# Kernel optimization log

Hardware: AMD Instinct MI355X
Metric: run time of the kernel (lower is better)

Reference implementation:

```python
import jax, jax.numpy as jnp
import numpy as np

N, E, F_IN, H, C = 20000, 320000, 256, 4, 64
D = H * C  # hidden_dim = 256
NEG_SLOPE = 0.2
LN_EPS = 1e-5


def setup_inputs() -> dict:
    key = jax.random.key(0)
    ks = jax.random.split(key, 12)
    x = jax.random.normal(ks[0], (N, F_IN), dtype=jnp.float32)
    # edges guaranteed self-loop-free (PyG GATConv removes then re-adds self loops)
    dst = jax.random.randint(ks[1], (E,), 0, N)
    off = jax.random.randint(ks[2], (E,), 1, N)
    src = (dst + off) % N
    edge_index = jnp.stack([src, dst]).astype(jnp.int64)

    def lin(k, fan_in, shape):
        return jax.random.normal(k, shape, dtype=jnp.float32) / np.sqrt(fan_in)

    W1 = lin(ks[3], F_IN, (F_IN, D)); b1 = jnp.zeros((D,), jnp.float32)
    a_src1 = lin(ks[4], C, (H, C)); a_dst1 = lin(ks[5], C, (H, C))
    W2 = lin(ks[6], D, (D, D)); b2 = jnp.zeros((D,), jnp.float32)
    a_src2 = lin(ks[7], C, (H, C)); a_dst2 = lin(ks[8], C, (H, C))
    g1 = jnp.ones((D,), jnp.float32); be1 = jnp.zeros((D,), jnp.float32)
    g2 = jnp.ones((D,), jnp.float32); be2 = jnp.zeros((D,), jnp.float32)
    attn_w = lin(ks[9], D, (D, 1)); attn_b = jnp.zeros((1,), jnp.float32)
    return dict(x=x, edge_index=edge_index, W1=W1, b1=b1, a_src1=a_src1,
                a_dst1=a_dst1, W2=W2, b2=b2, a_src2=a_src2, a_dst2=a_dst2,
                g1=g1, be1=be1, g2=g2, be2=be2, attn_w=attn_w, attn_b=attn_b)


def _gat_conv(x, src, dst, W, b, a_src, a_dst):
    # x: [N, F] -> h: [N, H, C]
    h = (x @ W).reshape(N, H, C)
    alpha_s = jnp.einsum('nhc,hc->nh', h, a_src)  # [N, H]
    alpha_d = jnp.einsum('nhc,hc->nh', h, a_dst)
    e = jax.nn.leaky_relu(alpha_s[src] + alpha_d[dst], NEG_SLOPE)  # [E', H]
    # segment softmax over edges sharing a destination
    m = jax.ops.segment_max(e, dst, num_segments=N)
    w = jnp.exp(e - m[dst])
    z = jax.ops.segment_sum(w, dst, num_segments=N)
    alpha = w / (z[dst] + 1e-16)
    out = jax.ops.segment_sum(h[src] * alpha[:, :, None], dst, num_segments=N)
    return out.reshape(N, D) + b


def _layernorm(x, g, b):
    mu = x.mean(-1, keepdims=True)
    var = ((x - mu) ** 2).mean(-1, keepdims=True)
    return (x - mu) * jax.lax.rsqrt(var + LN_EPS) * g + b


def reference(x, edge_index, W1, b1, a_src1, a_dst1, W2, b2, a_src2, a_dst2,
              g1, be1, g2, be2, attn_w, attn_b):
    loops = jnp.arange(N, dtype=edge_index.dtype)
    src = jnp.concatenate([edge_index[0], loops])
    dst = jnp.concatenate([edge_index[1], loops])
    x1 = _gat_conv(x, src, dst, W1, b1, a_src1, a_dst1)
    x1 = jax.nn.elu(_layernorm(x1, g1, be1))
    x2 = _gat_conv(x1, src, dst, W2, b2, a_src2, a_dst2)
    x2 = jax.nn.elu(_layernorm(x2, g2, be2) + x1)
    attn = jax.nn.softmax(x2 @ attn_w + attn_b, axis=0)  # softmax over nodes
    pooled = (x2 * attn).sum(axis=0)  # [D]
    return pooled
```

## Files before the change

kernel.cpp:

```cpp
#include <hip/hip_runtime.h>
#include <math.h>

#define N_NODES 20000
#define E_EDGES 320000
#define TOT_E   (E_EDGES + N_NODES)
#define DHID    256
#define NHEAD   4
#define SCAN_NB ((N_NODES + 255) / 256)
#define SPART   32

typedef float f32x4 __attribute__((ext_vector_type(4)));
typedef short short8 __attribute__((ext_vector_type(8)));
typedef unsigned short ushort;

__device__ __forceinline__ float wave_sum(float v) {
#pragma unroll
  for (int off = 32; off; off >>= 1) v += __shfl_xor(v, off);
  return v;
}
__device__ __forceinline__ ushort f2bf(float f) {
  unsigned u = __float_as_uint(f);
  u += 0x7fffu + ((u >> 16) & 1u);
  return (ushort)(u >> 16);
}
__device__ __forceinline__ float bflo(unsigned u) {
  return __uint_as_float(u << 16);
}
__device__ __forceinline__ float bfhi(unsigned u) {
  return __uint_as_float(u & 0xffff0000u);
}

__global__ void hist_kernel(const int* __restrict__ ei, int* __restrict__ deg) {
  int e = blockIdx.x * blockDim.x + threadIdx.x;
  if (e >= TOT_E) return;
  int dst = (e < E_EDGES) ? ei[E_EDGES + e] : (e - E_EDGES);
  atomicAdd(&deg[dst], 1);
}

__global__ __launch_bounds__(256)
void scan_blocks_kernel(const int* __restrict__ deg, int* __restrict__ bsum) {
  __shared__ int ws[4];
  const int t = threadIdx.x;
  const int i = blockIdx.x * 256 + t;
  int v = (i < N_NODES) ? deg[i] : 0;
  int s = v;
#pragma unroll
  for (int off = 32; off; off >>= 1) s += __shfl_xor(s, off);
  if ((t & 63) == 0) ws[t >> 6] = s;
  __syncthreads();
  if (t == 0) bsum[blockIdx.x] = ws[0] + ws[1] + ws[2] + ws[3];
}

__global__ __launch_bounds__(128)
void scan_tops_kernel(const int* __restrict__ bsum, int* __restrict__ boff) {
  __shared__ int tmp[SCAN_NB];
  const int t = threadIdx.x;
  if (t < SCAN_NB) tmp[t] = bsum[t];
  __syncthreads();
  if (t == 0) {
    int run = 0;
    for (int i = 0; i < SCAN_NB; ++i) { int x = tmp[i]; tmp[i] = run; run += x; }
  }
  __syncthreads();
  if (t < SCAN_NB) boff[t] = tmp[t];
}

__global__ __launch_bounds__(256)
void scan_apply_kernel(const int* __restrict__ deg, const int* __restrict__ boff,
                       int* __restrict__ rowp, int* __restrict__ cur) {
  __shared__ int ws[4];
  const int t = threadIdx.x;
  const int lane = t & 63, w = t >> 6;
  const int i = blockIdx.x * 256 + t;
  int v = (i < N_NODES) ? deg[i] : 0;
  int inc = v;
#pragma unroll
  for (int off = 1; off < 64; off <<= 1) {
    int u = __shfl_up(inc, off);
    if (lane >= off) inc += u;
  }
  if (lane == 63) ws[w] = inc;
  __syncthreads();
  int add = boff[blockIdx.x];
#pragma unroll
  for (int k = 0; k < 4; ++k)
    if (k < w) add += ws[k];
  int exc = add + inc - v;
  if (i < N_NODES) {
    rowp[i] = exc;
    cur[i] = exc;
    if (i == N_NODES - 1) rowp[N_NODES] = exc + v;
  }
}

__global__ void scatter_kernel(const int* __restrict__ ei, int* __restrict__ cur,
                               int* __restrict__ colb) {
  int e = blockIdx.x * blockDim.x + threadIdx.x;
  if (e >= TOT_E) return;
  int src, dst;
  if (e < E_EDGES) { src = ei[e]; dst = ei[E_EDGES + e]; }
  else             { src = dst = e - E_EDGES; }
  int pos = atomicAdd(&cur[dst], 1);
  colb[pos] = src;
}

__global__ __launch_bounds__(256)
void conv_inputs_kernel(const float* __restrict__ W1, const float* __restrict__ W2,
                        const float* __restrict__ x, ushort* __restrict__ Wt1,
                        ushort* __restrict__ Wt2, ushort* __restrict__ xb,
                        int* __restrict__ deg) {
  const int b = blockIdx.x;
  if (b < 512) {
    const float* W = (b < 256) ? W1 : W2;
    ushort* Wt = (b < 256) ? Wt1 : Wt2;
    const int n = b & 255;
    const int k = threadIdx.x;
    Wt[n * 256 + k] = f2bf(W[k * 256 + n]);
  } else if (b < 512 + N_NODES * 256 / 8 / 256) {
    int idx = (b - 512) * 256 + threadIdx.x;
    size_t base = (size_t)idx * 8;
    float4 a = *reinterpret_cast<const float4*>(x + base);
    float4 c = *reinterpret_cast<const float4*>(x + base + 4);
    short8 o;
    o[0] = f2bf(a.x); o[1] = f2bf(a.y); o[2] = f2bf(a.z); o[3] = f2bf(a.w);
    o[4] = f2bf(c.x); o[5] = f2bf(c.y); o[6] = f2bf(c.z); o[7] = f2bf(c.w);
    *reinterpret_cast<short8*>(xb + base) = o;
  } else {
    int idx = (b - (512 + N_NODES * 256 / 8 / 256)) * 256 + threadIdx.x;
    if (idx < N_NODES) deg[idx] = 0;
  }
}

__global__ __launch_bounds__(256)
void gemm_alpha_kernel(const ushort* __restrict__ Ab, const ushort* __restrict__ Wt,
                       const float* __restrict__ asrc, const float* __restrict__ adst,
                       ushort* __restrict__ hout, float* __restrict__ as_,
                       float* __restrict__ ad_) {
  __shared__ ushort hs[32 * 256];

  const int t = threadIdx.x;
  const int w = t >> 6;
  const int l = t & 63;
  const int row0 = blockIdx.x * 32;

  const ushort* abase = Ab + (size_t)(row0 + (l & 15)) * 256 + ((l >> 4) * 8);
  const ushort* bbase = Wt + (size_t)(w * 64 + (l & 15)) * 256 + ((l >> 4) * 8);

  f32x4 acc[2][4];
#pragma unroll
  for (int i = 0; i < 2; ++i)
#pragma unroll
    for (int j = 0; j < 4; ++j) acc[i][j] = (f32x4){0.f, 0.f, 0.f, 0.f};

  short8 a0 = *reinterpret_cast<const short8*>(abase);
  short8 a1 = *reinterpret_cast<const short8*>(abase + 16 * 256);
  short8 b0 = *reinterpret_cast<const short8*>(bbase);
  short8 b1 = *reinterpret_cast<const short8*>(bbase + 16 * 256);
  short8 b2 = *reinterpret_cast<const short8*>(bbase + 32 * 256);
  short8 b3 = *reinterpret_cast<const short8*>(bbase + 48 * 256);
#pragma unroll
  for (int kk = 0; kk < 256; kk += 32) {
    short8 na0, na1, nb0, nb1, nb2, nb3;
    if (kk + 32 < 256) {
      na0 = *reinterpret_cast<const short8*>(abase + kk + 32);
      na1 = *reinterpret_cast<const short8*>(abase + 16 * 256 + kk + 32);
      nb0 = *reinterpret_cast<const short8*>(bbase + kk + 32);
      nb1 = *reinterpret_cast<const short8*>(bbase + 16 * 256 + kk + 32);
      nb2 = *reinterpret_cast<const short8*>(bbase + 32 * 256 + kk + 32);
      nb3 = *reinterpret_cast<const short8*>(bbase + 48 * 256 + kk + 32);
    }
    acc[0][0] = __builtin_amdgcn_mfma_f32_16x16x32_bf16(a0, b0, acc[0][0], 0, 0, 0);
    acc[0][1] = __builtin_amdgcn_mfma_f32_16x16x32_bf16(a0, b1, acc[0][1], 0, 0, 0);
    acc[0][2] = __builtin_amdgcn_mfma_f32_16x16x32_bf16(a0, b2, acc[0][2], 0, 0, 0);
    acc[0][3] = __builtin_amdgcn_mfma_f32_16x16x32_bf16(a0, b3, acc[0][3], 0, 0, 0);
    acc[1][0] = __builtin_amdgcn_mfma_f32_16x16x32_bf16(a1, b0, acc[1][0], 0, 0, 0);
    acc[1][1] = __builtin_amdgcn_mfma_f32_16x16x32_bf16(a1, b1, acc[1][1], 0, 0, 0);
    acc[1][2] = __builtin_amdgcn_mfma_f32_16x16x32_bf16(a1, b2, acc[1][2], 0, 0, 0);
    acc[1][3] = __builtin_amdgcn_mfma_f32_16x16x32_bf16(a1, b3, acc[1][3], 0, 0, 0);
    if (kk + 32 < 256) {
      a0 = na0; a1 = na1; b0 = nb0; b1 = nb1; b2 = nb2; b3 = nb3;
    }
  }

  float asj[4], adj[4];
#pragma unroll
  for (int j = 0; j < 4; ++j) {
    asj[j] = asrc[w * 64 + j * 16 + (l & 15)];
    adj[j] = adst[w * 64 + j * 16 + (l & 15)];
  }
#pragma unroll
  for (int i = 0; i < 2; ++i) {
#pragma unroll
    for (int q = 0; q < 4; ++q) {
      float ps = 0.f, pd = 0.f;
#pragma unroll
      for (int j = 0; j < 4; ++j) {
        ps += acc[i][j][q] * asj[j];
        pd += acc[i][j][q] * adj[j];
      }
#pragma unroll
      for (int off = 1; off < 16; off <<= 1) {
        ps += __shfl_xor(ps, off);
        pd += __shfl_xor(pd, off);
      }
      int row = row0 + i * 16 + (l >> 4) * 4 + q;
      if ((l & 15) == 0) {
        as_[row * 4 + w] = ps;
        ad_[row * 4 + w] = pd;
      }
    }
  }

#pragma unroll
  for (int i = 0; i < 2; ++i)
#pragma unroll
    for (int j = 0; j < 4; ++j)
#pragma unroll
      for (int q = 0; q < 4; ++q) {
        int row = i * 16 + (l >> 4) * 4 + q;
        int col = w * 64 + j * 16 + (l & 15);
        hs[row * 256 + col] = f2bf(acc[i][j][q]);
      }
  __syncthreads();
#pragma unroll
  for (int g = 0; g < 4; ++g) {
    int gi = g * 256 + t;
    int row = gi >> 5;
    int slot = gi & 31;
    *reinterpret_cast<short8*>(hout + (size_t)(row0 + row) * 256 + slot * 8) =
        *reinterpret_cast<const short8*>(&hs[row * 256 + slot * 8]);
  }
}

__global__ __launch_bounds__(256)
void attn_gather_ln_kernel(const ushort* __restrict__ h, const float* __restrict__ as_,
                           const float* __restrict__ ad_, const int* __restrict__ rowp,
                           const int* __restrict__ colb, const float* __restrict__ bias,
                           const float* __restrict__ gamma, const float* __restrict__ beta,
                           const ushort* __restrict__ residb, ushort* __restrict__ outb,
                           const float* __restrict__ aw, const float* __restrict__ ab,
                           float* __restrict__ score) {
  const int t = threadIdx.x;
  const int d = blockIdx.x * 4 + (t >> 6);
  const int l = t & 63;
  const int start = rowp[d];
  const int deg = rowp[d + 1] - start;

  const int e16 = l >> 2, hh = l & 3;
  const float adv = ad_[d * 4 + hh];
  float M = -INFINITY;
  for (int i = e16; i < deg; i += 16) {
    int s = colb[start + i];
    float e = as_[s * 4 + hh] + adv;
    e = (e >= 0.f) ? e : 0.2f * e;
    M = fmaxf(M, e);
  }
#pragma unroll
  for (int off = 4; off < 64; off <<= 1) M = fmaxf(M, __shfl_xor(M, off));

  const int gh = l >> 4;
  const float Mg = __shfl(M, gh);
  const float adg = __shfl(adv, gh);

  float a0 = 0.f, a1 = 0.f, a2 = 0.f, a3 = 0.f, z = 0.f;
  const int c0 = l * 4;
  const ushort* hrow = h + c0;
#pragma unroll 2
  for (int i = 0; i < deg; ++i) {
    int s = colb[start + i];
    float e = as_[s * 4 + gh] + adg;
    e = (e >= 0.f) ? e : 0.2f * e;
    float wv = __expf(e - Mg);
    z += wv;
    uint2 hv = *reinterpret_cast<const uint2*>(hrow + (size_t)s * 256);
    a0 += wv * bflo(hv.x);
    a1 += wv * bfhi(hv.x);
    a2 += wv * bflo(hv.y);
    a3 += wv * bfhi(hv.y);
  }
  const float zi = 1.f / (z + 1e-16f);
  float4 bi = *reinterpret_cast<const float4*>(bias + c0);
  float v0 = a0 * zi + bi.x, v1 = a1 * zi + bi.y;
  float v2 = a2 * zi + bi.z, v3 = a3 * zi + bi.w;

  float s1 = wave_sum(v0 + v1 + v2 + v3);
  float s2 = wave_sum(v0 * v0 + v1 * v1 + v2 * v2 + v3 * v3);
  float mu = s1 * (1.f / 256.f);
  float var = s2 * (1.f / 256.f) - mu * mu;
  float rstd = rsqrtf(var + 1e-5f);
  float4 ga = *reinterpret_cast<const float4*>(gamma + c0);
  float4 be = *reinterpret_cast<const float4*>(beta + c0);
  float y0 = (v0 - mu) * rstd * ga.x + be.x;
  float y1 = (v1 - mu) * rstd * ga.y + be.y;
  float y2 = (v2 - mu) * rstd * ga.z + be.z;
  float y3 = (v3 - mu) * rstd * ga.w + be.w;
  if (residb) {
    uint2 rv = *reinterpret_cast<const uint2*>(residb + (size_t)d * 256 + c0);
    y0 += bflo(rv.x); y1 += bfhi(rv.x); y2 += bflo(rv.y); y3 += bfhi(rv.y);
  }
  y0 = (y0 > 0.f) ? y0 : expm1f(y0);
  y1 = (y1 > 0.f) ? y1 : expm1f(y1);
  y2 = (y2 > 0.f) ? y2 : expm1f(y2);
  y3 = (y3 > 0.f) ? y3 : expm1f(y3);

  uint2 o;
  o.x = ((unsigned)f2bf(y0)) | (((unsigned)f2bf(y1)) << 16);
  o.y = ((unsigned)f2bf(y2)) | (((unsigned)f2bf(y3)) << 16);
  *reinterpret_cast<uint2*>(outb + (size_t)d * 256 + c0) = o;

  if (score) {
    float4 aww = *reinterpret_cast<const float4*>(aw + c0);
    float sp = wave_sum(y0 * aww.x + y1 * aww.y + y2 * aww.z + y3 * aww.w);
    if (l == 0) score[d] = sp + ab[0];
  }
}

__global__ __launch_bounds__(256)
void score_part_kernel(const float* __restrict__ s, float* __restrict__ pm,
                       float* __restrict__ pz) {
  __shared__ float red[4];
  const int t = threadIdx.x, b = blockIdx.x;
  const int lane = t & 63, wid = t >> 6;
  float m = -INFINITY;
  for (int n = b * 256 + t; n < N_NODES; n += SPART * 256) m = fmaxf(m, s[n]);
#pragma unroll
  for (int off = 32; off; off >>= 1) m = fmaxf(m, __shfl_xor(m, off));
  if (lane == 0) red[wid] = m;
  __syncthreads();
  m = fmaxf(fmaxf(red[0], red[1]), fmaxf(red[2], red[3]));
  __syncthreads();
  float z = 0.f;
  for (int n = b * 256 + t; n < N_NODES; n += SPART * 256) z += __expf(s[n] - m);
  z = wave_sum(z);
  if (lane == 0) red[wid] = z;
  __syncthreads();
  if (t == 0) { pm[b] = m; pz[b] = red[0] + red[1] + red[2] + red[3]; }
}

__global__ __launch_bounds__(64)
void score_comb_kernel(const float* __restrict__ pm, const float* __restrict__ pz,
                       float* __restrict__ mz) {
  const int l = threadIdx.x;
  float m = (l < SPART) ? pm[l] : -INFINITY;
#pragma unroll
  for (int off = 32; off; off >>= 1) m = fmaxf(m, __shfl_xor(m, off));
  float z = (l < SPART) ? pz[l] * __expf(pm[l] - m) : 0.f;
  z = wave_sum(z);
  if (l == 0) { mz[0] = m; mz[1] = z; }
}

__global__ __launch_bounds__(256)
void pool_partial_kernel(const ushort* __restrict__ hb2, const float* __restrict__ s,
                         const float* __restrict__ mz, float* __restrict__ part) {
  __shared__ float red4[4][256];
  const int t = threadIdx.x, b = blockIdx.x;
  const int c4 = t & 63, rsub = t >> 6;
  const float m = mz[0];
  const float invz = 1.f / mz[1];
  f32x4 acc = (f32x4){0.f, 0.f, 0.f, 0.f};
  for (int n = b * 4 + rsub; n < N_NODES; n += 1024) {
    float w = __expf(s[n] - m);
    uint2 hv = *reinterpret_cast<const uint2*>(hb2 + (size_t)n * 256 + c4 * 4);
    acc[0] += w * bflo(hv.x);
    acc[1] += w * bfhi(hv.x);
    acc[2] += w * bflo(hv.y);
    acc[3] += w * bfhi(hv.y);
  }
#pragma unroll
  for (int k = 0; k < 4; ++k) red4[rsub][c4 * 4 + k] = acc[k];
  __syncthreads();
  if (t < 256) {
    float v = red4[0][t] + red4[1][t] + red4[2][t] + red4[3][t];
    part[b * 256 + t] = v * invz;
  }
}

__global__ __launch_bounds__(256)
void pool_final_kernel(const float* __restrict__ part, float* __restrict__ out) {
  const int t = threadIdx.x;
  float acc = 0.f;
  for (int b = 0; b < 256; ++b) acc += part[b * 256 + t];
  out[t] = acc;
}

extern "C" void kernel_launch(void* const* d_in, const int* in_sizes, int n_in,
                              void* d_out, int out_size, void* d_ws, size_t ws_size,
                              hipStream_t stream) {
  const float* x      = (const float*)d_in[0];
  const int*   ei     = (const int*)d_in[1];
  const float* W1     = (const float*)d_in[2];
  const float* b1     = (const float*)d_in[3];
  const float* a_src1 = (const float*)d_in[4];
  const float* a_dst1 = (const float*)d_in[5];
  const float* W2     = (const float*)d_in[6];
  const float* b2     = (const float*)d_in[7];
  const float* a_src2 = (const float*)d_in[8];
  const float* a_dst2 = (const float*)d_in[9];
  const float* g1     = (const float*)d_in[10];
  const float* be1    = (const float*)d_in[11];
  const float* g2     = (const float*)d_in[12];
  const float* be2    = (const float*)d_in[13];
  const float* attn_w = (const float*)d_in[14];
  const float* attn_b = (const float*)d_in[15];
  float* out = (float*)d_out;

  char* p = (char*)d_ws;
  auto alloc = [&](size_t bytes) {
    char* r = p;
    p += (bytes + 255) & ~size_t(255);
    return r;
  };
  ushort* h   = (ushort*)alloc((size_t)N_NODES * 256 * 2);
  ushort* xb  = (ushort*)alloc((size_t)N_NODES * 256 * 2);
  ushort* xb1 = (ushort*)alloc((size_t)N_NODES * 256 * 2);
  ushort* hb2 = (ushort*)alloc((size_t)N_NODES * 256 * 2);
  float* as_  = (float*)alloc((size_t)N_NODES * 4 * 4);
  float* ad_  = (float*)alloc((size_t)N_NODES * 4 * 4);
  float* sbuf = (float*)alloc((size_t)N_NODES * 4);
  float* mz   = (float*)alloc(256);
  float* pm   = (float*)alloc((size_t)SPART * 4);
  float* pz   = (float*)alloc((size_t)SPART * 4);
  float* part = (float*)alloc((size_t)256 * 256 * 4);
  ushort* wt1 = (ushort*)alloc((size_t)256 * 256 * 2);
  ushort* wt2 = (ushort*)alloc((size_t)256 * 256 * 2);
  int* deg    = (int*)alloc((size_t)N_NODES * 4);
  int* rowp   = (int*)alloc((size_t)(N_NODES + 1) * 4);
  int* cur    = (int*)alloc((size_t)N_NODES * 4);
  int* colb   = (int*)alloc((size_t)TOT_E * 4);
  int* bsum   = (int*)alloc((size_t)SCAN_NB * 4);
  int* boff   = (int*)alloc((size_t)SCAN_NB * 4);

  const int EB = (TOT_E + 255) / 256;
  const int GB = N_NODES / 32;
  const int DB = N_NODES / 4;
  const int XB = N_NODES * 256 / 8 / 256;
  const int CONVB = 512 + XB + SCAN_NB;

  conv_inputs_kernel<<<CONVB, 256, 0, stream>>>(W1, W2, x, wt1, wt2, xb, deg);
  hist_kernel<<<EB, 256, 0, stream>>>(ei, deg);
  scan_blocks_kernel<<<SCAN_NB, 256, 0, stream>>>(deg, bsum);
  scan_tops_kernel<<<1, 128, 0, stream>>>(bsum, boff);
  scan_apply_kernel<<<SCAN_NB, 256, 0, stream>>>(deg, boff, rowp, cur);
  scatter_kernel<<<EB, 256, 0, stream>>>(ei, cur, colb);

  gemm_alpha_kernel<<<GB, 256, 0, stream>>>(xb, wt1, a_src1, a_dst1, h, as_, ad_);
  attn_gather_ln_kernel<<<DB, 256, 0, stream>>>(h, as_, ad_, rowp, colb, b1, g1, be1,
                                                nullptr, xb1, nullptr, nullptr, nullptr);
  gemm_alpha_kernel<<<GB, 256, 0, stream>>>(xb1, wt2, a_src2, a_dst2, h, as_, ad_);
  attn_gather_ln_kernel<<<DB, 256, 0, stream>>>(h, as_, ad_, rowp, colb, b2, g2, be2,
                                                xb1, hb2, attn_w, attn_b, sbuf);
  score_part_kernel<<<SPART, 256, 0, stream>>>(sbuf, pm, pz);
  score_comb_kernel<<<1, 64, 0, stream>>>(pm, pz, mz);
  pool_partial_kernel<<<256, 256, 0, stream>>>(hb2, sbuf, mz, part);
  pool_final_kernel<<<1, 256, 0, stream>>>(part, out);
}
```

Baseline: 194.0 us.

## Drop softmax max pass and stage per-edge weights in LDS for gather

Removes the separate segment-max pass. Each edge's exp weight per head is now computed once, cooperatively across the wave, and staged with source indices in shared memory. The feature gather then reads weights from LDS and is unrolled four edges at a time to keep more loads in flight. This cuts redundant index, logit and exp work that every lane used to repeat. The cost is that an upper clamp at 60 replaces max subtraction, so very large or very negative logits could overflow or underflow differently from a true stable softmax. It also relies on wave-local LDS ordering without a barrier.

```diff
diff --git a/kernel.cpp b/kernel.cpp
--- a/kernel.cpp
+++ b/kernel.cpp
@@ -8,6 +8,7 @@
 #define NHEAD   4
 #define SCAN_NB ((N_NODES + 255) / 256)
 #define SPART   32
+#define ECAP    128
 
 typedef float f32x4 __attribute__((ext_vector_type(4)));
 typedef short short8 __attribute__((ext_vector_type(8)));
@@ -240,45 +241,68 @@
                            const ushort* __restrict__ residb, ushort* __restrict__ outb,
                            const float* __restrict__ aw, const float* __restrict__ ab,
                            float* __restrict__ score) {
-  const int t = threadIdx.x;
-  const int d = blockIdx.x * 4 + (t >> 6);
+  __shared__ float ew[4][ECAP][NHEAD];
+  __shared__ int   sidx[4][ECAP];
+
+  const int t = threadIdx.x;
+  const int wd = t >> 6;
+  const int d = blockIdx.x * 4 + wd;
   const int l = t & 63;
   const int start = rowp[d];
   const int deg = rowp[d + 1] - start;
+  const int* cb = colb + start;
 
   const int e16 = l >> 2, hh = l & 3;
   const float adv = ad_[d * 4 + hh];
-  float M = -INFINITY;
-  for (int i = e16; i < deg; i += 16) {
-    int s = colb[start + i];
-    float e = as_[s * 4 + hh] + adv;
-    e = (e >= 0.f) ? e : 0.2f * e;
-    M = fmaxf(M, e);
-  }
-#pragma unroll
-  for (int off = 4; off < 64; off <<= 1) M = fmaxf(M, __shfl_xor(M, off));
-
   const int gh = l >> 4;
-  const float Mg = __shfl(M, gh);
-  const float adg = __shfl(adv, gh);
-
-  float a0 = 0.f, a1 = 0.f, a2 = 0.f, a3 = 0.f, z = 0.f;
   const int c0 = l * 4;
   const ushort* hrow = h + c0;
-#pragma unroll 2
-  for (int i = 0; i < deg; ++i) {
-    int s = colb[start + i];
-    float e = as_[s * 4 + gh] + adg;
-    e = (e >= 0.f) ? e : 0.2f * e;
-    float wv = __expf(e - Mg);
-    z += wv;
-    uint2 hv = *reinterpret_cast<const uint2*>(hrow + (size_t)s * 256);
-    a0 += wv * bflo(hv.x);
-    a1 += wv * bfhi(hv.x);
-    a2 += wv * bflo(hv.y);
-    a3 += wv * bfhi(hv.y);
-  }
-  const float zi = 1.f / (z + 1e-16f);
+
+  float zpart = 0.f;
+  float a0 = 0.f, a1 = 0.f, a2 = 0.f, a3 = 0.f;
+
+  for (int base = 0; base < deg; base += ECAP) {
+    const int cnt = min(deg - base, ECAP);
+    for (int i = e16; i < cnt; i += 16) {
+      int s = cb[base + i];
+      if (hh == 0) sidx[wd][i] = s;
+      float e = as_[s * 4 + hh] + adv;
+      e = (e >= 0.f) ? e : 0.2f * e;
+      e = fminf(e, 60.f);
+      float wv = __expf(e);
+      ew[wd][i][hh] = wv;
+      zpart += wv;
+    }
+    int i = 0;
+    for (; i + 4 <= cnt; i += 4) {
+      int s0 = sidx[wd][i], s1 = sidx[wd][i + 1];
+      int s2 = sidx[wd][i + 2], s3 = sidx[wd][i + 3];
+      float w0 = ew[wd][i][gh], w1 = ew[wd][i + 1][gh];
+      float w2 = ew[wd][i + 2][gh], w3 = ew[wd][i + 3][gh];
+      uint2 h0 = *reinterpret_cast<const uint2*>(hrow + (size_t)s0 * 256);
+      uint2 h1 = *reinterpret_cast<const uint2*>(hrow + (size_t)s1 * 256);
+      uint2 h2 = *reinterpret_cast<const uint2*>(hrow + (size_t)s2 * 256);
+      uint2 h3 = *reinterpret_cast<const uint2*>(hrow + (size_t)s3 * 256);
+      a0 += w0 * bflo(h0.x) + w1 * bflo(h1.x) + w2 * bflo(h2.x) + w3 * bflo(h3.x);
+      a1 += w0 * bfhi(h0.x) + w1 * bfhi(h1.x) + w2 * bfhi(h2.x) + w3 * bfhi(h3.x);
+      a2 += w0 * bflo(h0.y) + w1 * bflo(h1.y) + w2 * bflo(h2.y) + w3 * bflo(h3.y);
+      a3 += w0 * bfhi(h0.y) + w1 * bfhi(h1.y) + w2 * bfhi(h2.y) + w3 * bfhi(h3.y);
+    }
+    for (; i < cnt; ++i) {
+      int s = sidx[wd][i];
+      float wv = ew[wd][i][gh];
+      uint2 hv = *reinterpret_cast<const uint2*>(hrow + (size_t)s * 256);
+      a0 += wv * bflo(hv.x);
+      a1 += wv * bfhi(hv.x);
+      a2 += wv * bflo(hv.y);
+      a3 += wv * bfhi(hv.y);
+    }
+  }
+
+#pragma unroll
+  for (int off = 4; off < 64; off <<= 1) zpart += __shfl_xor(zpart, off);
+  const float zi = 1.f / (__shfl(zpart, gh) + 1e-16f);
+
   float4 bi = *reinterpret_cast<const float4*>(bias + c0);
   float v0 = a0 * zi + bi.x, v1 = a1 * zi + bi.y;
   float v2 = a2 * zi + bi.z, v3 = a3 * zi + bi.w;
```

Measured after the change: 173.6 us. 10.5% less time.
